# Kernel tuning notes

Hardware: AMD Instinct MI355X
Metric: run time of the kernel (lower is better)

## Reference

```python
import jax, jax.numpy as jnp
import numpy as np

K = 3  # knn interpolation neighbors (init kwarg k)
EPS = 1e-8


def _knn_interpolate(x, pos, pos_skip, B, k):
    # Uniform per-batch counts (guaranteed by setup_inputs) let us vectorize the
    # per-batch cdist+topk+gather chain as batched dense ops.
    Nc = pos.shape[0] // B
    Nf = pos_skip.shape[0] // B
    C = x.shape[1]
    pc = pos.reshape(B, Nc, 3)        # coarse positions
    pf = pos_skip.reshape(B, Nf, 3)   # fine (target) positions
    xc = x.reshape(B, Nc, C)          # coarse features
    # squared pairwise distances via gemm: [B, Nf, Nc]
    d2 = (jnp.sum(pf * pf, -1)[:, :, None]
          + jnp.sum(pc * pc, -1)[:, None, :]
          - 2.0 * jnp.einsum('bfd,bcd->bfc', pf, pc))
    _, idx = jax.lax.top_k(-d2, k)    # k nearest coarse indices per fine point
    b = jnp.arange(B)[:, None, None]
    nb_pos = pc[b, idx]                              # [B,Nf,k,3]
    diff = nb_pos - pf[:, :, None, :]
    dist = jnp.sqrt(jnp.sum(diff * diff, -1))        # exact same dist math as torch
    w = 1.0 / (dist + EPS)                           # [B,Nf,k]
    feats = xc[b, idx]                               # [B,Nf,k,C]
    num = jnp.einsum('bfkc,bfk->bfc', feats, w)
    den = jnp.sum(w, -1, keepdims=True) + EPS
    return (num / den).reshape(B * Nf, C)


def setup_inputs() -> dict:
    key = jax.random.key(0)
    ks = jax.random.split(key, 6)
    B, Nc, Nf, C, Cs, H = 16, 1024, 4096, 512, 256, 512
    x = jax.random.normal(ks[0], (B * Nc, C), jnp.float32)
    pos = jax.random.normal(ks[1], (B * Nc, 3), jnp.float32)
    batch = jnp.repeat(jnp.arange(B, dtype=jnp.int64), Nc)
    x_skip = jax.random.normal(ks[2], (B * Nf, Cs), jnp.float32)
    pos_skip = jax.random.normal(ks[3], (B * Nf, 3), jnp.float32)
    batch_skip = jnp.repeat(jnp.arange(B, dtype=jnp.int64), Nf)
    # MLP params (self.nn = MLP 768 -> 512 -> 512, ReLU)
    W1 = jax.random.normal(ks[4], (C + Cs, H), jnp.float32) / np.sqrt(C + Cs).astype(np.float32)
    b1 = jnp.zeros((H,), jnp.float32)
    W2 = jax.random.normal(ks[5], (H, H), jnp.float32) / np.sqrt(H).astype(np.float32)
    b2 = jnp.zeros((H,), jnp.float32)
    return dict(x=x, pos=pos, batch=batch, x_skip=x_skip, pos_skip=pos_skip,
                batch_skip=batch_skip, W1=W1, b1=b1, W2=W2, b2=b2)


def reference(x, pos, batch, x_skip, pos_skip, batch_skip, W1, b1, W2, b2):
    B = int(np.asarray(batch).max()) + 1
    h = _knn_interpolate(x, pos, pos_skip, B, K)   # [N_fine, C]
    h = jnp.concatenate([h, x_skip], axis=1)       # skip connection concat
    h = jax.nn.relu(h @ W1 + b1)
    h = jax.nn.relu(h @ W2 + b2)
    return h
```

## Files before the change

### kernel.cpp

```cpp
#include <hip/hip_runtime.h>
#include <stdint.h>

typedef __attribute__((ext_vector_type(8))) short short8;
typedef __attribute__((ext_vector_type(4))) float f32x4;

static __device__ __forceinline__ ushort f2bf(float f) {
  uint32_t u = __float_as_uint(f);
  uint32_t r = (u + 0x7FFFu + ((u >> 16) & 1u)) >> 16;
  return (ushort)r;
}
static __device__ __forceinline__ float bf2f(ushort h) {
  return __uint_as_float(((uint32_t)h) << 16);
}

static __device__ __forceinline__ void ins3b(double d, int i,
    double& b0, double& b1, double& b2, int& i0, int& i1, int& i2) {
  const bool c0 = d < b0, c1 = d < b1, c2 = d < b2;
  const double nb0 = c0 ? d : b0;
  const int    ni0 = c0 ? i : i0;
  const double nb1 = c0 ? b0 : (c1 ? d : b1);
  const int    ni1 = c0 ? i0 : (c1 ? i : i1);
  const double nb2 = c1 ? b1 : (c2 ? d : b2);
  const int    ni2 = c1 ? i1 : (c2 ? i : i2);
  b0 = nb0; b1 = nb1; b2 = nb2; i0 = ni0; i1 = ni1; i2 = ni2;
}

__global__ __launch_bounds__(256) void prep_kernel(
    const float* __restrict__ pos, const float* __restrict__ pos_skip,
    const float* __restrict__ x, const float* __restrict__ xs,
    const float* __restrict__ W1, const float* __restrict__ W2,
    int4* __restrict__ idx_out, float4* __restrict__ w_out,
    ushort* __restrict__ xbf, ushort* __restrict__ xsbf,
    ushort* __restrict__ W1at, ushort* __restrict__ W1bt,
    ushort* __restrict__ W2t)
{
  __shared__ float pc4[4096];
  if (blockIdx.x < 1024) {
    const int b   = blockIdx.x >> 6;
    const int blk = blockIdx.x & 63;
    for (int i = threadIdx.x; i < 1024; i += 256) {
      const float* ps = pos + (size_t)b * 3072 + i * 3;
      float4 v = { ps[0], ps[1], ps[2], 0.f };
      *(float4*)&pc4[i * 4] = v;
    }
    __syncthreads();

    const int p   = threadIdx.x >> 2;
    const int sub = threadIdx.x & 3;
    const int row = b * 4096 + blk * 64 + p;
    const float pxf = pos_skip[(size_t)row * 3 + 0];
    const float pyf = pos_skip[(size_t)row * 3 + 1];
    const float pzf = pos_skip[(size_t)row * 3 + 2];

    uint32_t c0 = 0xFFFFFFFFu, c1 = 0xFFFFFFFFu, c2 = 0xFFFFFFFFu, c3 = 0xFFFFFFFFu;
    auto ins4u = [&](uint32_t k) {
      const bool l0 = k < c0, l1 = k < c1, l2 = k < c2, l3 = k < c3;
      const uint32_t n0 = l0 ? k  : c0;
      const uint32_t n1 = l0 ? c0 : (l1 ? k : c1);
      const uint32_t n2 = l1 ? c1 : (l2 ? k : c2);
      const uint32_t n3 = l2 ? c2 : (l3 ? k : c3);
      c0 = n0; c1 = n1; c2 = n2; c3 = n3;
    };
#pragma unroll 4
    for (int j = 0; j < 256; ++j) {
      const int i = j * 4 + sub;
      const float4 q = *(const float4*)&pc4[i * 4];
      const float dx = q.x - pxf;
      const float dy = q.y - pyf;
      const float dz = q.z - pzf;
      const float d = fmaf(dx, dx, fmaf(dy, dy, dz * dz));
      ins4u((__float_as_uint(d) & 0xFFFFFC00u) | (uint32_t)i);
    }
#pragma unroll
    for (int m = 1; m <= 2; m <<= 1) {
      const uint32_t e0 = (uint32_t)__shfl_xor((int)c0, m);
      const uint32_t e1 = (uint32_t)__shfl_xor((int)c1, m);
      const uint32_t e2 = (uint32_t)__shfl_xor((int)c2, m);
      const uint32_t e3 = (uint32_t)__shfl_xor((int)c3, m);
      ins4u(e0); ins4u(e1); ins4u(e2); ins4u(e3);
    }
    if (sub == 0) {
      const double pxd = (double)pxf, pyd = (double)pyf, pzd = (double)pzf;
      auto exd = [&](int i) -> double {
        const double dx = (double)pc4[i * 4 + 0] - pxd;
        const double dy = (double)pc4[i * 4 + 1] - pyd;
        const double dz = (double)pc4[i * 4 + 2] - pzd;
        return dx * dx + dy * dy + dz * dz;
      };
      const int j0 = (int)(c0 & 1023u), j1 = (int)(c1 & 1023u);
      const int j2 = (int)(c2 & 1023u), j3 = (int)(c3 & 1023u);
      double b0 = 1e300, b1 = 1e300, b2 = 1e300;
      int i0 = 0, i1 = 0, i2 = 0;
      ins3b(exd(j0), j0, b0, b1, b2, i0, i1, i2);
      ins3b(exd(j1), j1, b0, b1, b2, i0, i1, i2);
      ins3b(exd(j2), j2, b0, b1, b2, i0, i1, i2);
      ins3b(exd(j3), j3, b0, b1, b2, i0, i1, i2);
      const double w0 = 1.0 / (sqrt(b0) + 1e-8);
      const double w1 = 1.0 / (sqrt(b1) + 1e-8);
      const double w2 = 1.0 / (sqrt(b2) + 1e-8);
      const double den = w0 + w1 + w2 + 1e-8;
      idx_out[row] = make_int4(i0, i1, i2, 0);
      w_out[row] = make_float4((float)(w0 / den), (float)(w1 / den), (float)(w2 / den), 0.f);
    }
  } else if (blockIdx.x < 3072) {
    const int id = (blockIdx.x - 1024) * 256 + threadIdx.x;
#pragma unroll
    for (int it = 0; it < 4; ++it) {
      const int i = id + it * 524288;
      const float4 v = *(const float4*)(x + (size_t)i * 4);
      ushort4 o = { f2bf(v.x), f2bf(v.y), f2bf(v.z), f2bf(v.w) };
      *(ushort4*)(xbf + (size_t)i * 4) = o;
    }
  } else if (blockIdx.x < 7168) {
    const int id = (blockIdx.x - 3072) * 256 + threadIdx.x;
#pragma unroll
    for (int it = 0; it < 4; ++it) {
      const int i = id + it * 1048576;
      const float4 v = *(const float4*)(xs + (size_t)i * 4);
      ushort4 o = { f2bf(v.x), f2bf(v.y), f2bf(v.z), f2bf(v.w) };
      *(ushort4*)(xsbf + (size_t)i * 4) = o;
    }
  } else {
    const int id = (blockIdx.x - 7168) * 256 + threadIdx.x;
    if (id < 262144) {
      const int n = id >> 9, k = id & 511;
      W1at[id] = f2bf(W1[(size_t)k * 512 + n]);
    } else if (id < 393216) {
      const int id2 = id - 262144;
      const int n = id2 >> 8, k = id2 & 255;
      W1bt[id2] = f2bf(W1[(size_t)(512 + k) * 512 + n]);
    } else if (id < 655360) {
      const int id3 = id - 393216;
      const int n = id3 >> 9, k = id3 & 511;
      W2t[id3] = f2bf(W2[(size_t)k * 512 + n]);
    }
  }
}

struct Y4 { short8 y0, y1, y2, s; };

__global__ __launch_bounds__(256) void combine_kernel(
    const ushort* __restrict__ Ybf, const ushort* __restrict__ S,
    const int4* __restrict__ idx3, const float4* __restrict__ w3,
    const float* __restrict__ b1, ushort* __restrict__ h2)
{
  const int xcd  = blockIdx.x & 7;
  const int j    = blockIdx.x >> 3;
  const int widx = j * 4 + (threadIdx.x >> 6);
  const int lane = threadIdx.x & 63;
  const int rbase = xcd * 8192 + widx * 4;

  const float4 bA = *(const float4*)(b1 + lane * 8);
  const float4 bB = *(const float4*)(b1 + lane * 8 + 4);

  int4   ids[4];
  float4 wts[4];
#pragma unroll
  for (int k = 0; k < 4; ++k) { ids[k] = idx3[rbase + k]; wts[k] = w3[rbase + k]; }

  const ushort* Yb = Ybf + (size_t)(rbase >> 12) * 524288;

  Y4 r0, r1, r2, r3;
  auto loadr = [&](int k, Y4& r) {
    r.y0 = *(const short8*)(Yb + (size_t)ids[k].x * 512 + lane * 8);
    r.y1 = *(const short8*)(Yb + (size_t)ids[k].y * 512 + lane * 8);
    r.y2 = *(const short8*)(Yb + (size_t)ids[k].z * 512 + lane * 8);
    r.s  = *(const short8*)(S + (size_t)(rbase + k) * 512 + lane * 8);
  };
  loadr(0, r0); loadr(1, r1); loadr(2, r2); loadr(3, r3);
  __builtin_amdgcn_sched_barrier(0);

  auto comp = [&](int k, const Y4& r) {
    const float4 w = wts[k];
    short8 o;
#pragma unroll
    for (int e = 0; e < 8; ++e) {
      const float be = (e < 4) ? ((const float*)&bA)[e] : ((const float*)&bB)[e - 4];
      float v = w.x * bf2f((ushort)r.y0[e])
              + w.y * bf2f((ushort)r.y1[e])
              + w.z * bf2f((ushort)r.y2[e])
              + bf2f((ushort)r.s[e]) + be;
      v = v > 0.f ? v : 0.f;
      o[e] = (short)f2bf(v);
    }
    *(short8*)(h2 + (size_t)(rbase + k) * 512 + lane * 8) = o;
  };
  comp(0, r0); comp(1, r1); comp(2, r2); comp(3, r3);
}

template<int K, bool OUT_BF16, bool ACT>
__global__ __launch_bounds__(512, 2) void gemm_bias_relu(
    const ushort* __restrict__ A, const ushort* __restrict__ Bt,
    const float* __restrict__ bias, void* __restrict__ Cout, int M, int N)
{
  constexpr int BM = 256, BN = 256, BK = 64, NT = K / BK;
  __shared__ ushort Asm[2][BM * BK];
  __shared__ ushort Bsm[2][BN * BK];
  const int tid  = threadIdx.x;
  const int lane = tid & 63;
  const int wave = tid >> 6;

  const int cpx  = gridDim.x >> 3;
  const int wgid = (blockIdx.x & 7) * cpx + (blockIdx.x >> 3);
  const int nbn  = N / BN;
  const int bm   = wgid / nbn;
  const int bn   = wgid - bm * nbn;
  const int row0 = bm * BM, col0 = bn * BN;
  const int wr = wave >> 2, wc = wave & 3;
  const int sbase = wave * 4096 + lane * 16;

  f32x4 acc[8][4] = {};

  auto stageA = [&](int buf, int kt) {
#pragma unroll
    for (int i = 0; i < 4; ++i) {
      const int o = sbase + i * 1024;
      const int r = o >> 7, s = (o & 127) >> 4;
      __builtin_amdgcn_global_load_lds(
          (const __attribute__((address_space(1))) void*)(A + (size_t)(row0 + r) * K + kt * BK + ((s ^ (r & 7)) << 3)),
          (__attribute__((address_space(3))) void*)((char*)&Asm[buf][0] + o), 16, 0, 0);
    }
  };
  auto stageB = [&](int buf, int kt) {
#pragma unroll
    for (int i = 0; i < 4; ++i) {
      const int o = sbase + i * 1024;
      const int r = o >> 7, s = (o & 127) >> 4;
      __builtin_amdgcn_global_load_lds(
          (const __attribute__((address_space(1))) void*)(Bt + (size_t)(col0 + r) * K + kt * BK + ((s ^ (r & 7)) << 3)),
          (__attribute__((address_space(3))) void*)((char*)&Bsm[buf][0] + o), 16, 0, 0);
    }
  };
  auto rdA = [&](int buf, int mi, int kk) -> short8 {
    const int ra = wr * 128 + mi * 16 + (lane & 15);
    const int s  = kk * 4 + (lane >> 4);
    return *(const short8*)((const char*)&Asm[buf][0] + ra * 128 + ((s ^ (ra & 7)) << 4));
  };
  auto rdB = [&](int buf, int ni, int kk) -> short8 {
    const int rb = wc * 64 + ni * 16 + (lane & 15);
    const int s  = kk * 4 + (lane >> 4);
    return *(const short8*)((const char*)&Bsm[buf][0] + rb * 128 + ((s ^ (rb & 7)) << 4));
  };

  stageA(0, 0); stageB(0, 0);
  asm volatile("s_waitcnt vmcnt(0)" ::: "memory");
  __builtin_amdgcn_s_barrier();

  int cur = 0;
#pragma unroll 1
  for (int t = 0; t < NT; ++t) {
    short8 av[4], bv[4];
#pragma unroll
    for (int mi = 0; mi < 4; ++mi) av[mi] = rdA(cur, mi, 0);
#pragma unroll
    for (int ni = 0; ni < 4; ++ni) bv[ni] = rdB(cur, ni, 0);
    if (t + 1 < NT) stageA(cur ^ 1, t + 1);
    __builtin_amdgcn_s_barrier();
    asm volatile("s_waitcnt lgkmcnt(0)" ::: "memory");
    __builtin_amdgcn_sched_barrier(0);
    __builtin_amdgcn_s_setprio(1);
#pragma unroll
    for (int mi = 0; mi < 4; ++mi)
#pragma unroll
      for (int ni = 0; ni < 4; ++ni)
        acc[mi][ni] = __builtin_amdgcn_mfma_f32_16x16x32_bf16(av[mi], bv[ni], acc[mi][ni], 0, 0, 0);
    __builtin_amdgcn_s_setprio(0);
    __builtin_amdgcn_s_barrier();
#pragma unroll
    for (int mi = 0; mi < 4; ++mi) av[mi] = rdA(cur, 4 + mi, 0);
    if (t + 1 < NT) stageB(cur ^ 1, t + 1);
    __builtin_amdgcn_s_barrier();
    asm volatile("s_waitcnt lgkmcnt(0)" ::: "memory");
    __builtin_amdgcn_sched_barrier(0);
    __builtin_amdgcn_s_setprio(1);
#pragma unroll
    for (int mi = 0; mi < 4; ++mi)
#pragma unroll
      for (int ni = 0; ni < 4; ++ni)
        acc[4 + mi][ni] = __builtin_amdgcn_mfma_f32_16x16x32_bf16(av[mi], bv[ni], acc[4 + mi][ni], 0, 0, 0);
    __builtin_amdgcn_s_setprio(0);
    __builtin_amdgcn_s_barrier();
#pragma unroll
    for (int mi = 0; mi < 4; ++mi) av[mi] = rdA(cur, mi, 1);
#pragma unroll
    for (int ni = 0; ni < 4; ++ni) bv[ni] = rdB(cur, ni, 1);
    __builtin_amdgcn_s_barrier();
    asm volatile("s_waitcnt lgkmcnt(0)" ::: "memory");
    __builtin_amdgcn_sched_barrier(0);
    __builtin_amdgcn_s_setprio(1);
#pragma unroll
    for (int mi = 0; mi < 4; ++mi)
#pragma unroll
      for (int ni = 0; ni < 4; ++ni)
        acc[mi][ni] = __builtin_amdgcn_mfma_f32_16x16x32_bf16(av[mi], bv[ni], acc[mi][ni], 0, 0, 0);
    __builtin_amdgcn_s_setprio(0);
    __builtin_amdgcn_s_barrier();
#pragma unroll
    for (int mi = 0; mi < 4; ++mi) av[mi] = rdA(cur, 4 + mi, 1);
    __builtin_amdgcn_s_barrier();
    asm volatile("s_waitcnt lgkmcnt(0)" ::: "memory");
    __builtin_amdgcn_sched_barrier(0);
    __builtin_amdgcn_s_setprio(1);
#pragma unroll
    for (int mi = 0; mi < 4; ++mi)
#pragma unroll
      for (int ni = 0; ni < 4; ++ni)
        acc[4 + mi][ni] = __builtin_amdgcn_mfma_f32_16x16x32_bf16(av[mi], bv[ni], acc[4 + mi][ni], 0, 0, 0);
    __builtin_amdgcn_s_setprio(0);
    asm volatile("s_waitcnt vmcnt(0)" ::: "memory");
    __builtin_amdgcn_s_barrier();
    cur ^= 1;
  }

  const int lc = lane & 15, lr = lane >> 4;
#pragma unroll
  for (int mi = 0; mi < 8; ++mi) {
#pragma unroll
    for (int ni = 0; ni < 4; ++ni) {
      const int col = col0 + wc * 64 + ni * 16 + lc;
      float bv2 = 0.f;
      if constexpr (ACT) bv2 = bias[col];
      const int rbase = row0 + wr * 128 + mi * 16 + lr * 4;
#pragma unroll
      for (int r = 0; r < 4; ++r) {
        float v = acc[mi][ni][r];
        if constexpr (ACT) { v += bv2; v = v > 0.f ? v : 0.f; }
        if (OUT_BF16) ((ushort*)Cout)[(size_t)(rbase + r) * N + col] = f2bf(v);
        else          ((float*)Cout)[(size_t)(rbase + r) * N + col] = v;
      }
    }
  }
}

extern "C" void kernel_launch(void* const* d_in, const int* in_sizes, int n_in,
                              void* d_out, int out_size, void* d_ws, size_t ws_size,
                              hipStream_t stream) {
  const float* x        = (const float*)d_in[0];
  const float* pos      = (const float*)d_in[1];
  const float* x_skip   = (const float*)d_in[3];
  const float* pos_skip = (const float*)d_in[4];
  const float* W1       = (const float*)d_in[6];
  const float* b1       = (const float*)d_in[7];
  const float* W2       = (const float*)d_in[8];
  const float* b2       = (const float*)d_in[9];

  ushort* Ybf  = (ushort*)d_out;
  ushort* S    = (ushort*)((char*)d_out + 16777216);
  ushort* xbf  = (ushort*)((char*)d_out + 83886080);
  ushort* xsbf = (ushort*)((char*)d_out + 100663296);

  char* ws = (char*)d_ws;
  ushort* h2   = (ushort*)ws;
  ushort* W1at = (ushort*)(ws + 67108864);
  ushort* W1bt = (ushort*)(ws + 67633152);
  ushort* W2t  = (ushort*)(ws + 67895296);
  int4*   idx3 = (int4*)  (ws + 68419584);
  float4* w3   = (float4*)(ws + 69468160);

  prep_kernel<<<9728, 256, 0, stream>>>(pos, pos_skip, x, x_skip, W1, W2,
                                        idx3, w3, xbf, xsbf, W1at, W1bt, W2t);
  gemm_bias_relu<512, true, false><<<128, 512, 0, stream>>>(xbf, W1at, nullptr, (void*)Ybf, 16384, 512);
  gemm_bias_relu<256, true, false><<<512, 512, 0, stream>>>(xsbf, W1bt, nullptr, (void*)S, 65536, 512);
  combine_kernel<<<4096, 256, 0, stream>>>(Ybf, S, idx3, w3, b1, h2);
  gemm_bias_relu<512, false, true><<<512, 512, 0, stream>>>(h2, W2t, b2, d_out, 65536, 512);
}
```

Measured before the change: 174.1 us.

## Fuse KNN combine into skip-GEMM epilogue, drop intermediate S buffer

Removes the separate combine kernel by doing the weighted gather of the three neighbour rows of Y, the bias add and the ReLU inside the epilogue of the x_skip GEMM, which now writes h2 directly. This avoids writing the S tensor (64 MB of bf16) and reading it back, and saves one launch. In exchange the epilogue does scattered 2-byte gathers per element, with lanes reading 16 contiguous columns each. That may coalesce worse than the old 16-byte vectorized loads and adds register pressure to the GEMM kernel.

```diff
diff --git a/kernel.cpp b/kernel.cpp
--- a/kernel.cpp
+++ b/kernel.cpp
@@ -137,61 +137,12 @@
   }
 }
 
-struct Y4 { short8 y0, y1, y2, s; };
-
-__global__ __launch_bounds__(256) void combine_kernel(
-    const ushort* __restrict__ Ybf, const ushort* __restrict__ S,
-    const int4* __restrict__ idx3, const float4* __restrict__ w3,
-    const float* __restrict__ b1, ushort* __restrict__ h2)
-{
-  const int xcd  = blockIdx.x & 7;
-  const int j    = blockIdx.x >> 3;
-  const int widx = j * 4 + (threadIdx.x >> 6);
-  const int lane = threadIdx.x & 63;
-  const int rbase = xcd * 8192 + widx * 4;
-
-  const float4 bA = *(const float4*)(b1 + lane * 8);
-  const float4 bB = *(const float4*)(b1 + lane * 8 + 4);
-
-  int4   ids[4];
-  float4 wts[4];
-#pragma unroll
-  for (int k = 0; k < 4; ++k) { ids[k] = idx3[rbase + k]; wts[k] = w3[rbase + k]; }
-
-  const ushort* Yb = Ybf + (size_t)(rbase >> 12) * 524288;
-
-  Y4 r0, r1, r2, r3;
-  auto loadr = [&](int k, Y4& r) {
-    r.y0 = *(const short8*)(Yb + (size_t)ids[k].x * 512 + lane * 8);
-    r.y1 = *(const short8*)(Yb + (size_t)ids[k].y * 512 + lane * 8);
-    r.y2 = *(const short8*)(Yb + (size_t)ids[k].z * 512 + lane * 8);
-    r.s  = *(const short8*)(S + (size_t)(rbase + k) * 512 + lane * 8);
-  };
-  loadr(0, r0); loadr(1, r1); loadr(2, r2); loadr(3, r3);
-  __builtin_amdgcn_sched_barrier(0);
-
-  auto comp = [&](int k, const Y4& r) {
-    const float4 w = wts[k];
-    short8 o;
-#pragma unroll
-    for (int e = 0; e < 8; ++e) {
-      const float be = (e < 4) ? ((const float*)&bA)[e] : ((const float*)&bB)[e - 4];
-      float v = w.x * bf2f((ushort)r.y0[e])
-              + w.y * bf2f((ushort)r.y1[e])
-              + w.z * bf2f((ushort)r.y2[e])
-              + bf2f((ushort)r.s[e]) + be;
-      v = v > 0.f ? v : 0.f;
-      o[e] = (short)f2bf(v);
-    }
-    *(short8*)(h2 + (size_t)(rbase + k) * 512 + lane * 8) = o;
-  };
-  comp(0, r0); comp(1, r1); comp(2, r2); comp(3, r3);
-}
-
-template<int K, bool OUT_BF16, bool ACT>
+template<int K, bool OUT_BF16, bool ACT, bool COMBINE>
 __global__ __launch_bounds__(512, 2) void gemm_bias_relu(
     const ushort* __restrict__ A, const ushort* __restrict__ Bt,
-    const float* __restrict__ bias, void* __restrict__ Cout, int M, int N)
+    const float* __restrict__ bias, void* __restrict__ Cout, int M, int N,
+    const ushort* __restrict__ Ybf, const int4* __restrict__ idx3,
+    const float4* __restrict__ w3)
 {
   constexpr int BM = 256, BN = 256, BK = 64, NT = K / BK;
   __shared__ ushort Asm[2][BM * BK];
@@ -313,20 +264,47 @@
   }
 
   const int lc = lane & 15, lr = lane >> 4;
-#pragma unroll
-  for (int mi = 0; mi < 8; ++mi) {
-#pragma unroll
-    for (int ni = 0; ni < 4; ++ni) {
-      const int col = col0 + wc * 64 + ni * 16 + lc;
-      float bv2 = 0.f;
-      if constexpr (ACT) bv2 = bias[col];
-      const int rbase = row0 + wr * 128 + mi * 16 + lr * 4;
+  if constexpr (COMBINE) {
+#pragma unroll
+    for (int mi = 0; mi < 8; ++mi) {
 #pragma unroll
       for (int r = 0; r < 4; ++r) {
-        float v = acc[mi][ni][r];
-        if constexpr (ACT) { v += bv2; v = v > 0.f ? v : 0.f; }
-        if (OUT_BF16) ((ushort*)Cout)[(size_t)(rbase + r) * N + col] = f2bf(v);
-        else          ((float*)Cout)[(size_t)(rbase + r) * N + col] = v;
+        const int row = row0 + wr * 128 + mi * 16 + lr * 4 + r;
+        const int4 id = idx3[row];
+        const float4 w = w3[row];
+        const ushort* Yb = Ybf + (size_t)(row >> 12) * 524288;
+        const ushort* y0 = Yb + (size_t)id.x * 512;
+        const ushort* y1 = Yb + (size_t)id.y * 512;
+        const ushort* y2 = Yb + (size_t)id.z * 512;
+#pragma unroll
+        for (int ni = 0; ni < 4; ++ni) {
+          const int col = col0 + wc * 64 + ni * 16 + lc;
+          float v = acc[mi][ni][r]
+                  + w.x * bf2f(y0[col])
+                  + w.y * bf2f(y1[col])
+                  + w.z * bf2f(y2[col])
+                  + bias[col];
+          v = v > 0.f ? v : 0.f;
+          ((ushort*)Cout)[(size_t)row * 512 + col] = f2bf(v);
+        }
+      }
+    }
+  } else {
+#pragma unroll
+    for (int mi = 0; mi < 8; ++mi) {
+#pragma unroll
+      for (int ni = 0; ni < 4; ++ni) {
+        const int col = col0 + wc * 64 + ni * 16 + lc;
+        float bv2 = 0.f;
+        if constexpr (ACT) bv2 = bias[col];
+        const int rbase = row0 + wr * 128 + mi * 16 + lr * 4;
+#pragma unroll
+        for (int r = 0; r < 4; ++r) {
+          float v = acc[mi][ni][r];
+          if constexpr (ACT) { v += bv2; v = v > 0.f ? v : 0.f; }
+          if (OUT_BF16) ((ushort*)Cout)[(size_t)(rbase + r) * N + col] = f2bf(v);
+          else          ((float*)Cout)[(size_t)(rbase + r) * N + col] = v;
+        }
       }
     }
   }
@@ -345,7 +323,6 @@
   const float* b2       = (const float*)d_in[9];
 
   ushort* Ybf  = (ushort*)d_out;
-  ushort* S    = (ushort*)((char*)d_out + 16777216);
   ushort* xbf  = (ushort*)((char*)d_out + 83886080);
   ushort* xsbf = (ushort*)((char*)d_out + 100663296);
 
@@ -359,8 +336,10 @@
 
   prep_kernel<<<9728, 256, 0, stream>>>(pos, pos_skip, x, x_skip, W1, W2,
                                         idx3, w3, xbf, xsbf, W1at, W1bt, W2t);
-  gemm_bias_relu<512, true, false><<<128, 512, 0, stream>>>(xbf, W1at, nullptr, (void*)Ybf, 16384, 512);
-  gemm_bias_relu<256, true, false><<<512, 512, 0, stream>>>(xsbf, W1bt, nullptr, (void*)S, 65536, 512);
-  combine_kernel<<<4096, 256, 0, stream>>>(Ybf, S, idx3, w3, b1, h2);
-  gemm_bias_relu<512, false, true><<<512, 512, 0, stream>>>(h2, W2t, b2, d_out, 65536, 512);
-}
+  gemm_bias_relu<512, true, false, false><<<128, 512, 0, stream>>>(
+      xbf, W1at, nullptr, (void*)Ybf, 16384, 512, nullptr, nullptr, nullptr);
+  gemm_bias_relu<256, true, false, true><<<512, 512, 0, stream>>>(
+      xsbf, W1bt, b1, (void*)h2, 65536, 512, Ybf, idx3, w3);
+  gemm_bias_relu<512, false, true, false><<<512, 512, 0, stream>>>(
+      h2, W2t, b2, d_out, 65536, 512, nullptr, nullptr, nullptr);
+}
```

New measurement: 168.8 us, median of 3. -3.0%, faster.
